# Optimization experiments

Measured on AMD Instinct MI355X. Metric: run time of the kernel, lower is better.

Reference implementation:

```python
import jax, jax.numpy as jnp
import numpy as np

N, D, K, E_T = 16384, 64, 3, 262144
EPS = 1e-8

def layernorm(x, g, b):
    m = x.mean(-1, keepdims=True)
    v = x.var(-1, keepdims=True)
    return (x - m) * jax.lax.rsqrt(v + 1e-5) * g + b

def knn_edges(coords, k):
    # PyG knn_graph(loop=False, flow='source_to_target'): edge (neighbor -> query)
    n = coords.shape[0]
    sq = jnp.sum(coords * coords, axis=-1)
    d = sq[:, None] + sq[None, :] - 2.0 * (coords @ coords.T)  # [N,N] sq dists
    d = d.at[jnp.arange(n), jnp.arange(n)].set(jnp.inf)  # exclude self
    _, idx = jax.lax.top_k(-d, k)  # [N,k] nearest neighbor indices
    src = idx.reshape(-1)
    dst = jnp.repeat(jnp.arange(n), k)
    return src, dst

def gcn_conv(x, W, b, src, dst, ew, n):
    h = x @ W
    deg = jax.ops.segment_sum(ew, dst, num_segments=n)
    dis = jnp.where(deg > 0, jax.lax.rsqrt(jnp.maximum(deg, EPS)), 0.0)
    norm = dis[src] * ew * dis[dst]
    out = jax.ops.segment_sum(h[src] * norm[:, None], dst, num_segments=n)
    return out + b

def setup_inputs():
    key = jax.random.key(0)
    ks = jax.random.split(key, 8)
    return {
        "sp_center_feat": jax.random.normal(ks[0], (N, D), jnp.float32),
        "edge_index_tran": jax.random.randint(ks[1], (2, E_T), 0, N),
        "edge_attr_rpe": jax.random.normal(ks[2], (E_T, 3), jnp.float32),
        "norm_index": jax.random.randint(ks[3], (2,), 0, N),
        "sp_crood": jax.random.uniform(ks[4], (N, 3), jnp.float32),
        "norm1_g": jnp.ones((D,), jnp.float32), "norm1_b": jnp.zeros((D,), jnp.float32),
        "norm2_g": jnp.ones((D,), jnp.float32), "norm2_b": jnp.zeros((D,), jnp.float32),
        "gcn_norm_g": jnp.ones((D,), jnp.float32), "gcn_norm_b": jnp.zeros((D,), jnp.float32),
        "W1": jax.random.normal(ks[5], (D, D), jnp.float32) / np.sqrt(D),
        "b1": jnp.zeros((D,), jnp.float32),
        "W2": jax.random.normal(ks[6], (D, D), jnp.float32) / np.sqrt(D),
        "b2": jnp.zeros((D,), jnp.float32),
    }

def reference(sp_center_feat, edge_index_tran, edge_attr_rpe, norm_index, sp_crood,
              norm1_g, norm1_b, norm2_g, norm2_b, gcn_norm_g, gcn_norm_b,
              W1, b1, W2, b2):
    n = sp_center_feat.shape[0]
    x = layernorm(sp_center_feat, norm1_g, norm1_b)
    x = x + x  # SPgrah (external transformer) stubbed as identity; module adds shortcut
    x = layernorm(x, norm2_g, norm2_b)
    shortcut = x
    src, dst = knn_edges(sp_crood, K)
    a = x[src]; b_ = x[dst]
    na = jnp.maximum(jnp.sqrt(jnp.sum(a * a, -1)), EPS)
    nb = jnp.maximum(jnp.sqrt(jnp.sum(b_ * b_, -1)), EPS)
    ew_knn = jax.nn.sigmoid(jnp.sum(a * b_, -1) / (na * nb))  # sigmoid(cosine sim)
    loop = jnp.arange(n)
    src2 = jnp.concatenate([src, loop])
    dst2 = jnp.concatenate([dst, loop])
    ew = jnp.concatenate([ew_knn, jnp.ones((n,), ew_knn.dtype)])  # self-loops w=1
    h = gcn_conv(x, W1, b1, src2, dst2, ew, n)
    h = jax.nn.relu(layernorm(h, gcn_norm_g, gcn_norm_b))
    h = gcn_conv(h, W2, b2, src2, dst2, ew, n)
    h = h + x  # residual inside SuperpointGCN
    return shortcut + h
```

## Files before the change

### kernel.cpp

```cpp
#include <hip/hip_runtime.h>
#include <math.h>

#define N 16384
#define GC 8
#define NCELL (GC*GC*GC)

__device__ __forceinline__ float wsum(float v){
  #pragma unroll
  for(int m=32;m>0;m>>=1) v += __shfl_xor(v,m,64);
  return v;
}

__device__ __forceinline__ void lexins(float dd,int j2,
    float&D0,float&D1,float&D2,int&I0,int&I1,int&I2){
  bool lt0=(dd<D0)||((dd==D0)&&(j2<I0));
  bool lt1=(dd<D1)||((dd==D1)&&(j2<I1));
  bool lt2=(dd<D2)||((dd==D2)&&(j2<I2));
  float nD2=lt1?D1:(lt2?dd:D2); int nI2=lt1?I1:(lt2?j2:I2);
  float nD1=lt0?D0:(lt1?dd:D1); int nI1=lt0?I0:(lt1?j2:I1);
  float nD0=lt0?dd:D0;          int nI0=lt0?j2:I0;
  D0=nD0;D1=nD1;D2=nD2;I0=nI0;I1=nI1;I2=nI2;
}

__device__ __forceinline__ float refdist(float qx,float qy,float qz,float qs,float4 cv){
  float dot=__fmaf_rn(qz,cv.z,__fmaf_rn(qy,cv.y,__fmul_rn(qx,cv.x)));
  float sc =__fadd_rn(qs,cv.w);
  return __fmaf_rn(-2.0f,dot,sc);
}

__global__ __launch_bounds__(256) void ln_kernel(const float* __restrict__ in,
    const float* __restrict__ g1,const float* __restrict__ b1,
    const float* __restrict__ g2,const float* __restrict__ b2,
    const float* __restrict__ coords,
    float* __restrict__ x, float* __restrict__ xn, float4* __restrict__ c4,
    int* __restrict__ cnt){
  int wave=threadIdx.x>>6, lane=threadIdx.x&63;
  int row=blockIdx.x*4+wave;
  float v=in[row*64+lane];
  float m=wsum(v)*(1.0f/64.0f);
  float d=v-m;
  float var=wsum(d*d)*(1.0f/64.0f);
  float y=d*(1.0f/sqrtf(var+1e-5f))*g1[lane]+b1[lane];
  y=y+y;
  float m2=wsum(y)*(1.0f/64.0f);
  float d2=y-m2;
  float var2=wsum(d2*d2)*(1.0f/64.0f);
  float z=d2*(1.0f/sqrtf(var2+1e-5f))*g2[lane]+b2[lane];
  x[row*64+lane]=z;
  float s=wsum(z*z);
  if(lane==0){
    xn[row]=fmaxf(sqrtf(s),1e-8f);
    float a=coords[row*3+0],b=coords[row*3+1],c=coords[row*3+2];
    float sq=__fadd_rn(__fadd_rn(__fmul_rn(a,a),__fmul_rn(b,b)),__fmul_rn(c,c));
    c4[row]=make_float4(a,b,c,sq);
    int cx=min(GC-1,(int)(a*(float)GC)), cy=min(GC-1,(int)(b*(float)GC)),
        cz=min(GC-1,(int)(c*(float)GC));
    atomicAdd(&cnt[(cz*GC+cy)*GC+cx],1);
  }
}

__global__ __launch_bounds__(256) void scatter_k(const float4* __restrict__ c4,
    const int* __restrict__ cnt, int* __restrict__ cursor,
    float4* __restrict__ sc4, int* __restrict__ sidx, int* __restrict__ cellSt){
  __shared__ int buf[NCELL];
  int tid=threadIdx.x;
  int c0v=cnt[tid], c1v=cnt[tid+256];
  buf[tid]=c0v; buf[tid+256]=c1v;
  __syncthreads();
  #pragma unroll
  for(int off=1;off<NCELL;off<<=1){
    int v0=(tid>=off)?buf[tid-off]:0;
    int v1=(tid+256>=off)?buf[tid+256-off]:0;
    __syncthreads();
    buf[tid]+=v0; buf[tid+256]+=v1;
    __syncthreads();
  }
  int e0=buf[tid]-c0v, e1=buf[tid+256]-c1v;
  if(blockIdx.x==0){
    cellSt[tid]=e0; cellSt[tid+256]=e1;
    if(tid==0) cellSt[NCELL]=N;
  }
  __syncthreads();
  buf[tid]=e0; buf[tid+256]=e1;
  __syncthreads();
  int i=blockIdx.x*256+tid;
  float4 v=c4[i];
  int cx=min(GC-1,(int)(v.x*(float)GC)), cy=min(GC-1,(int)(v.y*(float)GC)),
      cz=min(GC-1,(int)(v.z*(float)GC));
  int cell=(cz*GC+cy)*GC+cx;
  int pos=buf[cell]+atomicAdd(&cursor[cell],1);
  sc4[pos]=v; sidx[pos]=i;
}

__global__ __launch_bounds__(256) void knn_ew(const float4* __restrict__ sc4,
    const int* __restrict__ sidx, const int* __restrict__ cellSt,
    const float4* __restrict__ c4, const float* __restrict__ x,
    const float* __restrict__ xn,
    int* __restrict__ knn, float* __restrict__ ew, float* __restrict__ dis){
  int tid=threadIdx.x, bid=blockIdx.x;
  int gt=bid*256+tid;
  int lane=tid&63;
  int slot=gt>>5, part=tid&31;

  float4 qv=sc4[slot]; int q=sidx[slot];
  float qx=qv.x,qy=qv.y,qz=qv.z,qs=qv.w;
  int cx=min(GC-1,(int)(qx*(float)GC)), cy=min(GC-1,(int)(qy*(float)GC)),
      cz=min(GC-1,(int)(qz*(float)GC));
  float D0=1e30f,D1=1e30f,D2=1e30f; int I0=0x7fffffff,I1=0x7fffffff,I2=0x7fffffff;
  int xlo=max(cx-1,0), xhi=min(cx+1,GC-1);
  const float cw=1.0f/(float)GC;
  float fy0=qy-(float)cy*cw, fy1=(float)(cy+1)*cw-qy;
  float fz0=qz-(float)cz*cw, fz1=(float)(cz+1)*cw-qz;
  const int OY[9]={0,-1,1, 0,0,-1, 1,-1,1};
  const int OZ[9]={0, 0,0,-1,1,-1,-1, 1,1};
  #pragma unroll 1
  for(int k=0;k<9;k++){
    int oy=OY[k], oz=OZ[k];
    int y2=cy+oy, z2=cz+oz;
    if(y2<0||y2>=GC||z2<0||z2>=GC) continue;
    if(k>0){
      float dy=(oy<0)?fy0:((oy>0)?fy1:0.0f);
      float dz=(oz<0)?fz0:((oz>0)?fz1:0.0f);
      float bnd=dy*dy+dz*dz;
      if(bnd>D2+1e-5f) continue;
    }
    int rowb=(z2*GC+y2)*GC;
    int p0=cellSt[rowb+xlo], p1=cellSt[rowb+xhi+1];
    for(int p=p0+part;p<p1;p+=32){
      float4 cv=sc4[p]; int j2=sidx[p];
      float dd=refdist(qx,qy,qz,qs,cv);
      dd=(j2==q)?1e30f:dd;
      lexins(dd,j2,D0,D1,D2,I0,I1,I2);
    }
  }
  #pragma unroll
  for(int m=1;m<32;m<<=1){
    float e0=__shfl_xor(D0,m),e1=__shfl_xor(D1,m),e2=__shfl_xor(D2,m);
    int   f0=__shfl_xor(I0,m),f1=__shfl_xor(I1,m),f2=__shfl_xor(I2,m);
    lexins(e0,f0,D0,D1,D2,I0,I1,I2);
    lexins(e1,f1,D0,D1,D2,I0,I1,I2);
    lexins(e2,f2,D0,D1,D2,I0,I1,I2);
  }
  bool flg=false;
  if(part==0){
    float mg=1e30f;
    mg=fminf(mg,(cx>0)?(qx-(float)(cx-1)*cw):1e30f);
    mg=fminf(mg,(cx<GC-1)?((float)(cx+2)*cw-qx):1e30f);
    mg=fminf(mg,(cy>0)?(qy-(float)(cy-1)*cw):1e30f);
    mg=fminf(mg,(cy<GC-1)?((float)(cy+2)*cw-qy):1e30f);
    mg=fminf(mg,(cz>0)?(qz-(float)(cz-1)*cw):1e30f);
    mg=fminf(mg,(cz<GC-1)?((float)(cz+2)*cw-qz):1e30f);
    float mg2=mg*mg*(1.0f-1e-5f);
    flg=!(D2<mg2);
  }
  unsigned long long mask=__ballot(flg);
  while(mask){
    int b=__ffsll((unsigned long long)mask)-1; mask&=mask-1;
    int qb=__shfl(q,b);
    float bx=__shfl(qx,b),by=__shfl(qy,b),bz=__shfl(qz,b),bs=__shfl(qs,b);
    float E0=1e30f,E1=1e30f,E2=1e30f; int F0=0x7fffffff,F1=0x7fffffff,F2=0x7fffffff;
    for(int j=lane;j<N;j+=64){
      float4 cv=c4[j];
      float dd=refdist(bx,by,bz,bs,cv);
      dd=(j==qb)?1e30f:dd;
      lexins(dd,j,E0,E1,E2,F0,F1,F2);
    }
    #pragma unroll
    for(int m=1;m<64;m<<=1){
      float e0=__shfl_xor(E0,m),e1=__shfl_xor(E1,m),e2=__shfl_xor(E2,m);
      int   f0=__shfl_xor(F0,m),f1=__shfl_xor(F1,m),f2=__shfl_xor(F2,m);
      lexins(e0,f0,E0,E1,E2,F0,F1,F2);
      lexins(e1,f1,E0,E1,E2,F0,F1,F2);
      lexins(e2,f2,E0,E1,E2,F0,F1,F2);
    }
    if(lane==b){ I0=F0; I1=F1; I2=F2; }
  }
  if(part==0){ knn[q*3+0]=I0; knn[q*3+1]=I1; knn[q*3+2]=I2; }

  for(int r=0;r<2;r++){
    int qi=__shfl(q,32*r);
    int s0=__shfl(I0,32*r), s1=__shfl(I1,32*r), s2=__shfl(I2,32*r);
    float xi=x[qi*64+lane];
    float xs0=x[s0*64+lane], xs1=x[s1*64+lane], xs2=x[s2*64+lane];
    float n0=xn[s0], n1=xn[s1], n2=xn[s2];
    float ni=xn[qi];
    float dt0=wsum(xs0*xi), dt1=wsum(xs1*xi), dt2=wsum(xs2*xi);
    float e0=1.f/(1.f+expf(-(dt0/(n0*ni))));
    float e1=1.f/(1.f+expf(-(dt1/(n1*ni))));
    float e2=1.f/(1.f+expf(-(dt2/(n2*ni))));
    if(lane==0){
      ew[qi*3+0]=e0; ew[qi*3+1]=e1; ew[qi*3+2]=e2;
      float ssum=((e0+e1)+e2);
      dis[qi]=1.f/sqrtf(ssum+1.0f);
    }
  }
}

__global__ __launch_bounds__(256) void agg1_w1(const float* __restrict__ x,
    const float* __restrict__ ew, const float* __restrict__ dis,
    const int* __restrict__ knn, const float* __restrict__ W1,
    const float* __restrict__ bb1, const float* __restrict__ gg,
    const float* __restrict__ gb, float* __restrict__ a1){
  __shared__ float rowbuf[4][64];
  int tid=threadIdx.x;
  int wave=tid>>6, lane=tid&63;
  float wcol[64];
  #pragma unroll
  for(int k=0;k<64;k++) wcol[k]=W1[k*64+lane];
  float bv=bb1[lane], gv=gg[lane], bv2=gb[lane];
  int nb=blockIdx.x*16+wave*4;
  float xrA,dAA,xsA0,xsA1,xsA2,wA0,wA1,wA2;
  float xrB,dBB,xsB0,xsB1,xsB2,wB0,wB1,wB2;
  {
    int i=nb;
    float di=dis[i]; dAA=di*di;
    xrA=x[i*64+lane];
    int s0=knn[i*3+0], s1=knn[i*3+1], s2=knn[i*3+2];
    xsA0=x[s0*64+lane]; xsA1=x[s1*64+lane]; xsA2=x[s2*64+lane];
    wA0=dis[s0]*ew[i*3+0]*di; wA1=dis[s1]*ew[i*3+1]*di; wA2=dis[s2]*ew[i*3+2]*di;
  }
  #pragma unroll
  for(int r=0;r<4;r++){
    if(r<3){
      int i=nb+r+1;
      float di=dis[i]; dBB=di*di;
      xrB=x[i*64+lane];
      int s0=knn[i*3+0], s1=knn[i*3+1], s2=knn[i*3+2];
      xsB0=x[s0*64+lane]; xsB1=x[s1*64+lane]; xsB2=x[s2*64+lane];
      wB0=dis[s0]*ew[i*3+0]*di; wB1=dis[s1]*ew[i*3+1]*di; wB2=dis[s2]*ew[i*3+2]*di;
    }
    float xa=xrA*dAA;
    xa=fmaf(xsA0,wA0,xa); xa=fmaf(xsA1,wA1,xa); xa=fmaf(xsA2,wA2,xa);
    rowbuf[wave][lane]=xa;
    const float4* rb=(const float4*)&rowbuf[wave][0];
    float acc=0.f;
    #pragma unroll
    for(int k4=0;k4<16;k4++){
      float4 av=rb[k4];
      acc=fmaf(av.x,wcol[k4*4+0],acc);
      acc=fmaf(av.y,wcol[k4*4+1],acc);
      acc=fmaf(av.z,wcol[k4*4+2],acc);
      acc=fmaf(av.w,wcol[k4*4+3],acc);
    }
    acc+=bv;
    float mu=wsum(acc)*(1.0f/64.0f);
    float dd=acc-mu;
    float var=wsum(dd*dd)*(1.0f/64.0f);
    float y=dd*(1.0f/sqrtf(var+1e-5f))*gv+bv2;
    a1[(nb+r)*64+lane]=fmaxf(y,0.0f);
    xrA=xrB; dAA=dBB;
    xsA0=xsB0; xsA1=xsB1; xsA2=xsB2;
    wA0=wB0; wA1=wB1; wA2=wB2;
  }
}

__global__ __launch_bounds__(256) void agg2_w2(const float* __restrict__ a1,
    const float* __restrict__ ew, const float* __restrict__ dis,
    const int* __restrict__ knn, const float* __restrict__ W2,
    const float* __restrict__ bb2, const float* __restrict__ x,
    float* __restrict__ out){
  __shared__ float rowbuf[4][64];
  int tid=threadIdx.x;
  int wave=tid>>6, lane=tid&63;
  float wcol[64];
  #pragma unroll
  for(int k=0;k<64;k++) wcol[k]=W2[k*64+lane];
  float bv=bb2[lane];
  int nb=blockIdx.x*16+wave*4;
  float xrA,dAA,xsA0,xsA1,xsA2,wA0,wA1,wA2;
  float xrB,dBB,xsB0,xsB1,xsB2,wB0,wB1,wB2;
  {
    int i=nb;
    float di=dis[i]; dAA=di*di;
    xrA=a1[i*64+lane];
    int s0=knn[i*3+0], s1=knn[i*3+1], s2=knn[i*3+2];
    xsA0=a1[s0*64+lane]; xsA1=a1[s1*64+lane]; xsA2=a1[s2*64+lane];
    wA0=dis[s0]*ew[i*3+0]*di; wA1=dis[s1]*ew[i*3+1]*di; wA2=dis[s2]*ew[i*3+2]*di;
  }
  #pragma unroll
  for(int r=0;r<4;r++){
    if(r<3){
      int i=nb+r+1;
      float di=dis[i]; dBB=di*di;
      xrB=a1[i*64+lane];
      int s0=knn[i*3+0], s1=knn[i*3+1], s2=knn[i*3+2];
      xsB0=a1[s0*64+lane]; xsB1=a1[s1*64+lane]; xsB2=a1[s2*64+lane];
      wB0=dis[s0]*ew[i*3+0]*di; wB1=dis[s1]*ew[i*3+1]*di; wB2=dis[s2]*ew[i*3+2]*di;
    }
    float aa=xrA*dAA;
    aa=fmaf(xsA0,wA0,aa); aa=fmaf(xsA1,wA1,aa); aa=fmaf(xsA2,wA2,aa);
    rowbuf[wave][lane]=aa;
    const float4* rb=(const float4*)&rowbuf[wave][0];
    float acc=0.f;
    #pragma unroll
    for(int k4=0;k4<16;k4++){
      float4 av=rb[k4];
      acc=fmaf(av.x,wcol[k4*4+0],acc);
      acc=fmaf(av.y,wcol[k4*4+1],acc);
      acc=fmaf(av.z,wcol[k4*4+2],acc);
      acc=fmaf(av.w,wcol[k4*4+3],acc);
    }
    acc+=bv;
    float xv=x[(nb+r)*64+lane];
    out[(nb+r)*64+lane]=(acc+xv)+xv;
    xrA=xrB; dAA=dBB;
    xsA0=xsB0; xsA1=xsB1; xsA2=xsB2;
    wA0=wB0; wA1=wB1; wA2=wB2;
  }
}

extern "C" void kernel_launch(void* const* d_in, const int* in_sizes, int n_in,
                              void* d_out, int out_size, void* d_ws, size_t ws_size,
                              hipStream_t stream){
  const float* feat  =(const float*)d_in[0];
  const float* coords=(const float*)d_in[4];
  const float* g1 =(const float*)d_in[5];
  const float* b1n=(const float*)d_in[6];
  const float* g2 =(const float*)d_in[7];
  const float* b2n=(const float*)d_in[8];
  const float* gg =(const float*)d_in[9];
  const float* gb =(const float*)d_in[10];
  const float* W1 =(const float*)d_in[11];
  const float* bb1=(const float*)d_in[12];
  const float* W2 =(const float*)d_in[13];
  const float* bb2=(const float*)d_in[14];
  float* out=(float*)d_out;

  char* ws=(char*)d_ws;
  size_t o=0;
  float*  x      =(float*) (ws+o); o+=(size_t)N*64*4;
  float*  a1     =(float*) (ws+o); o+=(size_t)N*64*4;
  float*  xn     =(float*) (ws+o); o+=(size_t)N*4;
  float*  ew     =(float*) (ws+o); o+=(size_t)N*3*4;
  float*  dis    =(float*) (ws+o); o+=(size_t)N*4;
  int*    knn    =(int*)   (ws+o); o+=(size_t)N*3*4;
  float4* c4     =(float4*)(ws+o); o+=(size_t)N*16;
  float4* sc4    =(float4*)(ws+o); o+=(size_t)N*16;
  int*    sidx   =(int*)   (ws+o); o+=(size_t)N*4;
  int*    cellSt =(int*)   (ws+o); o+=(size_t)(NCELL+1)*4;
  o=(o+255)&~(size_t)255;
  int*    cnt    =(int*)   (ws+o); o+=(size_t)NCELL*4;
  int*    cursor =(int*)   (ws+o); o+=(size_t)NCELL*4;
  (void)ws_size; (void)in_sizes; (void)n_in; (void)out_size;

  hipMemsetAsync((void*)cnt, 0, (size_t)2*NCELL*4, stream);
  hipLaunchKernelGGL(ln_kernel, dim3(N/4),   dim3(256), 0, stream, feat,g1,b1n,g2,b2n,coords,x,xn,c4,cnt);
  hipLaunchKernelGGL(scatter_k, dim3(N/256), dim3(256), 0, stream, c4,cnt,cursor,sc4,sidx,cellSt);
  hipLaunchKernelGGL(knn_ew,    dim3(2048),  dim3(256), 0, stream, sc4,sidx,cellSt,c4,x,xn,knn,ew,dis);
  hipLaunchKernelGGL(agg1_w1,   dim3(N/16),  dim3(256), 0, stream, x,ew,dis,knn,W1,bb1,gg,gb,a1);
  hipLaunchKernelGGL(agg2_w2,   dim3(N/16),  dim3(256), 0, stream, a1,ew,dis,knn,W2,bb2,x,out);
}
```

Before: 155.4 us.

## Fuse all stages into one cooperative persistent kernel with grid syncs

Replaces the memset plus five kernel launches with a single cooperative kernel of 512 blocks that runs layernorm, cell histogram/scan, scatter, grid kNN with edge weights, and both GCN layers, separated by grid.sync. The cell histogram and scan now run in one block using shared-memory atomics. The aim is to remove launch overhead and the gaps between kernels. The cost is serialized phases in one block, fewer threads per phase (the kNN and aggregation loops run several passes per wave), and the overhead of grid-wide barriers. It falls back to the old multi-kernel path if the cooperative launch fails.

```diff
diff --git a/kernel.cpp b/kernel.cpp
--- a/kernel.cpp
+++ b/kernel.cpp
@@ -1,9 +1,15 @@
 #include <hip/hip_runtime.h>
+#include <hip/hip_cooperative_groups.h>
 #include <math.h>
+
+namespace cg = cooperative_groups;
 
 #define N 16384
 #define GC 8
 #define NCELL (GC*GC*GC)
+#define NBLK 512
+#define NTHR 256
+#define NWAVE ((NBLK*NTHR)/64)
 
 __device__ __forceinline__ float wsum(float v){
   #pragma unroll
@@ -26,6 +32,283 @@
   float dot=__fmaf_rn(qz,cv.z,__fmaf_rn(qy,cv.y,__fmul_rn(qx,cv.x)));
   float sc =__fadd_rn(qs,cv.w);
   return __fmaf_rn(-2.0f,dot,sc);
+}
+
+__device__ __forceinline__ int cellOf(float4 v){
+  int cx=min(GC-1,(int)(v.x*(float)GC)), cy=min(GC-1,(int)(v.y*(float)GC)),
+      cz=min(GC-1,(int)(v.z*(float)GC));
+  return (cz*GC+cy)*GC+cx;
+}
+
+struct Params {
+  const float *feat,*coords,*g1,*b1,*g2,*b2,*gg,*gb,*W1,*bb1,*W2,*bb2;
+  float *out;
+  float *x,*a1,*xn,*ew,*dis;
+  int *knn; float4 *c4,*sc4; int *sidx,*cellSt,*cursor;
+};
+
+__global__ __launch_bounds__(256,2) void fused(Params P){
+  cg::grid_group grid = cg::this_grid();
+  int tid=threadIdx.x, bid=blockIdx.x;
+  int gtid=bid*NTHR+tid;
+  int lane=tid&63, wave=tid>>6;
+  int gwave=gtid>>6;
+  __shared__ float rowbuf[4][64];
+  __shared__ int smem[2*NCELL];
+
+  if(gtid<NCELL) P.cursor[gtid]=0;
+  #pragma unroll 1
+  for(int rr=0;rr<8;rr++){
+    int row=gwave*8+rr;
+    float v=P.feat[row*64+lane];
+    float m=wsum(v)*(1.0f/64.0f);
+    float d=v-m;
+    float var=wsum(d*d)*(1.0f/64.0f);
+    float y=d*(1.0f/sqrtf(var+1e-5f))*P.g1[lane]+P.b1[lane];
+    y=y+y;
+    float m2=wsum(y)*(1.0f/64.0f);
+    float d2=y-m2;
+    float var2=wsum(d2*d2)*(1.0f/64.0f);
+    float z=d2*(1.0f/sqrtf(var2+1e-5f))*P.g2[lane]+P.b2[lane];
+    P.x[row*64+lane]=z;
+    float s=wsum(z*z);
+    if(lane==0){
+      P.xn[row]=fmaxf(sqrtf(s),1e-8f);
+      float a=P.coords[row*3+0],b=P.coords[row*3+1],c=P.coords[row*3+2];
+      float sq=__fadd_rn(__fadd_rn(__fmul_rn(a,a),__fmul_rn(b,b)),__fmul_rn(c,c));
+      P.c4[row]=make_float4(a,b,c,sq);
+    }
+  }
+  grid.sync();
+
+  if(bid==0){
+    for(int i=tid;i<NCELL;i+=NTHR) smem[i]=0;
+    __syncthreads();
+    for(int i=tid;i<N;i+=NTHR){
+      atomicAdd(&smem[cellOf(P.c4[i])],1);
+    }
+    __syncthreads();
+    for(int i=tid;i<NCELL;i+=NTHR) smem[NCELL+i]=smem[i];
+    __syncthreads();
+    for(int off=1;off<NCELL;off<<=1){
+      int v0=(tid>=off)?smem[NCELL+tid-off]:0;
+      int v1=((tid+256)>=off)?smem[NCELL+tid+256-off]:0;
+      __syncthreads();
+      smem[NCELL+tid]+=v0; smem[NCELL+tid+256]+=v1;
+      __syncthreads();
+    }
+    P.cellSt[tid]    =smem[NCELL+tid]    -smem[tid];
+    P.cellSt[tid+256]=smem[NCELL+tid+256]-smem[tid+256];
+    if(tid==0) P.cellSt[NCELL]=N;
+  }
+  grid.sync();
+
+  if(gtid<N){
+    float4 v=P.c4[gtid];
+    int cell=cellOf(v);
+    int pos=P.cellSt[cell]+atomicAdd(&P.cursor[cell],1);
+    P.sc4[pos]=v; P.sidx[pos]=gtid;
+  }
+  grid.sync();
+
+  #pragma unroll 1
+  for(int pass=0;pass<4;pass++){
+    int slot=pass*4096+(gwave<<1)+(lane>>5);
+    int part=lane&31;
+    float4 qv=P.sc4[slot]; int q=P.sidx[slot];
+    float qx=qv.x,qy=qv.y,qz=qv.z,qs=qv.w;
+    int cx=min(GC-1,(int)(qx*(float)GC)), cy=min(GC-1,(int)(qy*(float)GC)),
+        cz=min(GC-1,(int)(qz*(float)GC));
+    float D0=1e30f,D1=1e30f,D2=1e30f; int I0=0x7fffffff,I1=0x7fffffff,I2=0x7fffffff;
+    int xlo=max(cx-1,0), xhi=min(cx+1,GC-1);
+    const float cw=1.0f/(float)GC;
+    float fy0=qy-(float)cy*cw, fy1=(float)(cy+1)*cw-qy;
+    float fz0=qz-(float)cz*cw, fz1=(float)(cz+1)*cw-qz;
+    const int OY[9]={0,-1,1, 0,0,-1, 1,-1,1};
+    const int OZ[9]={0, 0,0,-1,1,-1,-1, 1,1};
+    #pragma unroll 1
+    for(int k=0;k<9;k++){
+      int oy=OY[k], oz=OZ[k];
+      int y2=cy+oy, z2=cz+oz;
+      if(y2<0||y2>=GC||z2<0||z2>=GC) continue;
+      if(k>0){
+        float dy=(oy<0)?fy0:((oy>0)?fy1:0.0f);
+        float dz=(oz<0)?fz0:((oz>0)?fz1:0.0f);
+        float bnd=dy*dy+dz*dz;
+        if(bnd>D2+1e-5f) continue;
+      }
+      int rowb=(z2*GC+y2)*GC;
+      int p0=P.cellSt[rowb+xlo], p1=P.cellSt[rowb+xhi+1];
+      for(int p=p0+part;p<p1;p+=32){
+        float4 cv=P.sc4[p]; int j2=P.sidx[p];
+        float dd=refdist(qx,qy,qz,qs,cv);
+        dd=(j2==q)?1e30f:dd;
+        lexins(dd,j2,D0,D1,D2,I0,I1,I2);
+      }
+    }
+    #pragma unroll
+    for(int m=1;m<32;m<<=1){
+      float e0=__shfl_xor(D0,m),e1=__shfl_xor(D1,m),e2=__shfl_xor(D2,m);
+      int   f0=__shfl_xor(I0,m),f1=__shfl_xor(I1,m),f2=__shfl_xor(I2,m);
+      lexins(e0,f0,D0,D1,D2,I0,I1,I2);
+      lexins(e1,f1,D0,D1,D2,I0,I1,I2);
+      lexins(e2,f2,D0,D1,D2,I0,I1,I2);
+    }
+    bool flg=false;
+    if(part==0){
+      float mg=1e30f;
+      mg=fminf(mg,(cx>0)?(qx-(float)(cx-1)*cw):1e30f);
+      mg=fminf(mg,(cx<GC-1)?((float)(cx+2)*cw-qx):1e30f);
+      mg=fminf(mg,(cy>0)?(qy-(float)(cy-1)*cw):1e30f);
+      mg=fminf(mg,(cy<GC-1)?((float)(cy+2)*cw-qy):1e30f);
+      mg=fminf(mg,(cz>0)?(qz-(float)(cz-1)*cw):1e30f);
+      mg=fminf(mg,(cz<GC-1)?((float)(cz+2)*cw-qz):1e30f);
+      float mg2=mg*mg*(1.0f-1e-5f);
+      flg=!(D2<mg2);
+    }
+    unsigned long long mask=__ballot(flg);
+    while(mask){
+      int b=__ffsll((unsigned long long)mask)-1; mask&=mask-1;
+      int qb=__shfl(q,b);
+      float bx=__shfl(qx,b),by=__shfl(qy,b),bz=__shfl(qz,b),bs=__shfl(qs,b);
+      float E0=1e30f,E1=1e30f,E2=1e30f; int F0=0x7fffffff,F1=0x7fffffff,F2=0x7fffffff;
+      for(int j=lane;j<N;j+=64){
+        float4 cv=P.c4[j];
+        float dd=refdist(bx,by,bz,bs,cv);
+        dd=(j==qb)?1e30f:dd;
+        lexins(dd,j,E0,E1,E2,F0,F1,F2);
+      }
+      #pragma unroll
+      for(int m=1;m<64;m<<=1){
+        float e0=__shfl_xor(E0,m),e1=__shfl_xor(E1,m),e2=__shfl_xor(E2,m);
+        int   f0=__shfl_xor(F0,m),f1=__shfl_xor(F1,m),f2=__shfl_xor(F2,m);
+        lexins(e0,f0,E0,E1,E2,F0,F1,F2);
+        lexins(e1,f1,E0,E1,E2,F0,F1,F2);
+        lexins(e2,f2,E0,E1,E2,F0,F1,F2);
+      }
+      if(lane==b){ I0=F0; I1=F1; I2=F2; }
+    }
+    if(part==0){ P.knn[q*3+0]=I0; P.knn[q*3+1]=I1; P.knn[q*3+2]=I2; }
+
+    for(int r=0;r<2;r++){
+      int qi=__shfl(q,32*r);
+      int s0=__shfl(I0,32*r), s1=__shfl(I1,32*r), s2=__shfl(I2,32*r);
+      float xi=P.x[qi*64+lane];
+      float xs0=P.x[s0*64+lane], xs1=P.x[s1*64+lane], xs2=P.x[s2*64+lane];
+      float n0=P.xn[s0], n1=P.xn[s1], n2=P.xn[s2];
+      float ni=P.xn[qi];
+      float dt0=wsum(xs0*xi), dt1=wsum(xs1*xi), dt2=wsum(xs2*xi);
+      float e0=1.f/(1.f+expf(-(dt0/(n0*ni))));
+      float e1=1.f/(1.f+expf(-(dt1/(n1*ni))));
+      float e2=1.f/(1.f+expf(-(dt2/(n2*ni))));
+      if(lane==0){
+        P.ew[qi*3+0]=e0; P.ew[qi*3+1]=e1; P.ew[qi*3+2]=e2;
+        float ssum=((e0+e1)+e2);
+        P.dis[qi]=1.f/sqrtf(ssum+1.0f);
+      }
+    }
+  }
+  grid.sync();
+
+  {
+    float wcol[64];
+    #pragma unroll
+    for(int k=0;k<64;k++) wcol[k]=P.W1[k*64+lane];
+    float bv=P.bb1[lane], gv=P.gg[lane], bv2=P.gb[lane];
+    int nb=gwave*8;
+    float xrA,dAA,xsA0,xsA1,xsA2,wA0,wA1,wA2;
+    float xrB,dBB,xsB0,xsB1,xsB2,wB0,wB1,wB2;
+    {
+      int i=nb;
+      float di=P.dis[i]; dAA=di*di;
+      xrA=P.x[i*64+lane];
+      int s0=P.knn[i*3+0], s1=P.knn[i*3+1], s2=P.knn[i*3+2];
+      xsA0=P.x[s0*64+lane]; xsA1=P.x[s1*64+lane]; xsA2=P.x[s2*64+lane];
+      wA0=P.dis[s0]*P.ew[i*3+0]*di; wA1=P.dis[s1]*P.ew[i*3+1]*di; wA2=P.dis[s2]*P.ew[i*3+2]*di;
+    }
+    #pragma unroll 1
+    for(int r=0;r<8;r++){
+      if(r<7){
+        int i=nb+r+1;
+        float di=P.dis[i]; dBB=di*di;
+        xrB=P.x[i*64+lane];
+        int s0=P.knn[i*3+0], s1=P.knn[i*3+1], s2=P.knn[i*3+2];
+        xsB0=P.x[s0*64+lane]; xsB1=P.x[s1*64+lane]; xsB2=P.x[s2*64+lane];
+        wB0=P.dis[s0]*P.ew[i*3+0]*di; wB1=P.dis[s1]*P.ew[i*3+1]*di; wB2=P.dis[s2]*P.ew[i*3+2]*di;
+      }
+      float xa=xrA*dAA;
+      xa=fmaf(xsA0,wA0,xa); xa=fmaf(xsA1,wA1,xa); xa=fmaf(xsA2,wA2,xa);
+      rowbuf[wave][lane]=xa;
+      const float4* rb=(const float4*)&rowbuf[wave][0];
+      float acc=0.f;
+      #pragma unroll
+      for(int k4=0;k4<16;k4++){
+        float4 av=rb[k4];
+        acc=fmaf(av.x,wcol[k4*4+0],acc);
+        acc=fmaf(av.y,wcol[k4*4+1],acc);
+        acc=fmaf(av.z,wcol[k4*4+2],acc);
+        acc=fmaf(av.w,wcol[k4*4+3],acc);
+      }
+      acc+=bv;
+      float mu=wsum(acc)*(1.0f/64.0f);
+      float dd=acc-mu;
+      float var=wsum(dd*dd)*(1.0f/64.0f);
+      float y=dd*(1.0f/sqrtf(var+1e-5f))*gv+bv2;
+      P.a1[(nb+r)*64+lane]=fmaxf(y,0.0f);
+      xrA=xrB; dAA=dBB;
+      xsA0=xsB0; xsA1=xsB1; xsA2=xsB2;
+      wA0=wB0; wA1=wB1; wA2=wB2;
+    }
+  }
+  grid.sync();
+
+  {
+    float wcol[64];
+    #pragma unroll
+    for(int k=0;k<64;k++) wcol[k]=P.W2[k*64+lane];
+    float bv=P.bb2[lane];
+    int nb=gwave*8;
+    float xrA,dAA,xsA0,xsA1,xsA2,wA0,wA1,wA2;
+    float xrB,dBB,xsB0,xsB1,xsB2,wB0,wB1,wB2;
+    {
+      int i=nb;
+      float di=P.dis[i]; dAA=di*di;
+      xrA=P.a1[i*64+lane];
+      int s0=P.knn[i*3+0], s1=P.knn[i*3+1], s2=P.knn[i*3+2];
+      xsA0=P.a1[s0*64+lane]; xsA1=P.a1[s1*64+lane]; xsA2=P.a1[s2*64+lane];
+      wA0=P.dis[s0]*P.ew[i*3+0]*di; wA1=P.dis[s1]*P.ew[i*3+1]*di; wA2=P.dis[s2]*P.ew[i*3+2]*di;
+    }
+    #pragma unroll 1
+    for(int r=0;r<8;r++){
+      if(r<7){
+        int i=nb+r+1;
+        float di=P.dis[i]; dBB=di*di;
+        xrB=P.a1[i*64+lane];
+        int s0=P.knn[i*3+0], s1=P.knn[i*3+1], s2=P.knn[i*3+2];
+        xsB0=P.a1[s0*64+lane]; xsB1=P.a1[s1*64+lane]; xsB2=P.a1[s2*64+lane];
+        wB0=P.dis[s0]*P.ew[i*3+0]*di; wB1=P.dis[s1]*P.ew[i*3+1]*di; wB2=P.dis[s2]*P.ew[i*3+2]*di;
+      }
+      float aa=xrA*dAA;
+      aa=fmaf(xsA0,wA0,aa); aa=fmaf(xsA1,wA1,aa); aa=fmaf(xsA2,wA2,aa);
+      rowbuf[wave][lane]=aa;
+      const float4* rb=(const float4*)&rowbuf[wave][0];
+      float acc=0.f;
+      #pragma unroll
+      for(int k4=0;k4<16;k4++){
+        float4 av=rb[k4];
+        acc=fmaf(av.x,wcol[k4*4+0],acc);
+        acc=fmaf(av.y,wcol[k4*4+1],acc);
+        acc=fmaf(av.z,wcol[k4*4+2],acc);
+        acc=fmaf(av.w,wcol[k4*4+3],acc);
+      }
+      acc+=bv;
+      float xv=P.x[(nb+r)*64+lane];
+      P.out[(nb+r)*64+lane]=(acc+xv)+xv;
+      xrA=xrB; dAA=dBB;
+      xsA0=xsB0; xsA1=xsB1; xsA2=xsB2;
+      wA0=wB0; wA1=wB1; wA2=wB2;
+    }
+  }
 }
 
 __global__ __launch_bounds__(256) void ln_kernel(const float* __restrict__ in,
@@ -53,9 +336,7 @@
     float a=coords[row*3+0],b=coords[row*3+1],c=coords[row*3+2];
     float sq=__fadd_rn(__fadd_rn(__fmul_rn(a,a),__fmul_rn(b,b)),__fmul_rn(c,c));
     c4[row]=make_float4(a,b,c,sq);
-    int cx=min(GC-1,(int)(a*(float)GC)), cy=min(GC-1,(int)(b*(float)GC)),
-        cz=min(GC-1,(int)(c*(float)GC));
-    atomicAdd(&cnt[(cz*GC+cy)*GC+cx],1);
+    atomicAdd(&cnt[cellOf(make_float4(a,b,c,sq))],1);
   }
 }
 
@@ -85,9 +366,7 @@
   __syncthreads();
   int i=blockIdx.x*256+tid;
   float4 v=c4[i];
-  int cx=min(GC-1,(int)(v.x*(float)GC)), cy=min(GC-1,(int)(v.y*(float)GC)),
-      cz=min(GC-1,(int)(v.z*(float)GC));
-  int cell=(cz*GC+cy)*GC+cx;
+  int cell=cellOf(v);
   int pos=buf[cell]+atomicAdd(&cursor[cell],1);
   sc4[pos]=v; sidx[pos]=i;
 }
@@ -101,7 +380,6 @@
   int gt=bid*256+tid;
   int lane=tid&63;
   int slot=gt>>5, part=tid&31;
-
   float4 qv=sc4[slot]; int q=sidx[slot];
   float qx=qv.x,qy=qv.y,qz=qv.z,qs=qv.w;
   int cx=min(GC-1,(int)(qx*(float)GC)), cy=min(GC-1,(int)(qy*(float)GC)),
@@ -176,7 +454,6 @@
     if(lane==b){ I0=F0; I1=F1; I2=F2; }
   }
   if(part==0){ knn[q*3+0]=I0; knn[q*3+1]=I1; knn[q*3+2]=I2; }
-
   for(int r=0;r<2;r++){
     int qi=__shfl(q,32*r);
     int s0=__shfl(I0,32*r), s1=__shfl(I1,32*r), s2=__shfl(I2,32*r);
@@ -343,10 +620,22 @@
   int*    cursor =(int*)   (ws+o); o+=(size_t)NCELL*4;
   (void)ws_size; (void)in_sizes; (void)n_in; (void)out_size;
 
-  hipMemsetAsync((void*)cnt, 0, (size_t)2*NCELL*4, stream);
-  hipLaunchKernelGGL(ln_kernel, dim3(N/4),   dim3(256), 0, stream, feat,g1,b1n,g2,b2n,coords,x,xn,c4,cnt);
-  hipLaunchKernelGGL(scatter_k, dim3(N/256), dim3(256), 0, stream, c4,cnt,cursor,sc4,sidx,cellSt);
-  hipLaunchKernelGGL(knn_ew,    dim3(2048),  dim3(256), 0, stream, sc4,sidx,cellSt,c4,x,xn,knn,ew,dis);
-  hipLaunchKernelGGL(agg1_w1,   dim3(N/16),  dim3(256), 0, stream, x,ew,dis,knn,W1,bb1,gg,gb,a1);
-  hipLaunchKernelGGL(agg2_w2,   dim3(N/16),  dim3(256), 0, stream, a1,ew,dis,knn,W2,bb2,x,out);
-}
+  Params Pm;
+  Pm.feat=feat; Pm.coords=coords; Pm.g1=g1; Pm.b1=b1n; Pm.g2=g2; Pm.b2=b2n;
+  Pm.gg=gg; Pm.gb=gb; Pm.W1=W1; Pm.bb1=bb1; Pm.W2=W2; Pm.bb2=bb2;
+  Pm.out=out; Pm.x=x; Pm.a1=a1; Pm.xn=xn; Pm.ew=ew; Pm.dis=dis;
+  Pm.knn=knn; Pm.c4=c4; Pm.sc4=sc4; Pm.sidx=sidx; Pm.cellSt=cellSt; Pm.cursor=cursor;
+  void* args[] = { (void*)&Pm };
+
+  hipError_t e = hipLaunchCooperativeKernel((const void*)fused, dim3(NBLK), dim3(NTHR),
+                                            args, 0, stream);
+  if(e != hipSuccess){
+    (void)hipGetLastError();
+    hipMemsetAsync((void*)cnt, 0, (size_t)2*NCELL*4, stream);
+    hipLaunchKernelGGL(ln_kernel, dim3(N/4),   dim3(256), 0, stream, feat,g1,b1n,g2,b2n,coords,x,xn,c4,cnt);
+    hipLaunchKernelGGL(scatter_k, dim3(N/256), dim3(256), 0, stream, c4,cnt,cursor,sc4,sidx,cellSt);
+    hipLaunchKernelGGL(knn_ew,    dim3(2048),  dim3(256), 0, stream, sc4,sidx,cellSt,c4,x,xn,knn,ew,dis);
+    hipLaunchKernelGGL(agg1_w1,   dim3(N/16),  dim3(256), 0, stream, x,ew,dis,knn,W1,bb1,gg,gb,a1);
+    hipLaunchKernelGGL(agg2_w2,   dim3(N/16),  dim3(256), 0, stream, a1,ew,dis,knn,W2,bb2,x,out);
+  }
+}
```

After: 494.9 us. 218% more time.

## Fuse grid binning, scatter and layernorm into one launch, drop memset

Applied to the files above, without the earlier changes.

Merges the layernorm kernel and the cell-scatter kernel into a single launch. The first 64 blocks each recount all coordinates into shared-memory histograms, do a local prefix scan, and scatter their own points. The remaining blocks run the layernorm rows. This removes one kernel launch, the memset, and the global atomics. In exchange the scatter blocks do redundant work, each reading all 16384 coordinates with shared atomics, and the order of points within a cell becomes nondeterministic.

```diff
diff --git a/kernel.cpp b/kernel.cpp
--- a/kernel.cpp
+++ b/kernel.cpp
@@ -4,6 +4,8 @@
 #define N 16384
 #define GC 8
 #define NCELL (GC*GC*GC)
+#define NSCB (N/256)
+#define NLNB (N/4)
 
 __device__ __forceinline__ float wsum(float v){
   #pragma unroll
@@ -28,68 +30,73 @@
   return __fmaf_rn(-2.0f,dot,sc);
 }
 
-__global__ __launch_bounds__(256) void ln_kernel(const float* __restrict__ in,
+__device__ __forceinline__ int cellOf3(float a,float b,float c){
+  int cx=min(GC-1,(int)(a*(float)GC)), cy=min(GC-1,(int)(b*(float)GC)),
+      cz=min(GC-1,(int)(c*(float)GC));
+  return (cz*GC+cy)*GC+cx;
+}
+
+__global__ __launch_bounds__(256) void prep_ln(const float* __restrict__ in,
     const float* __restrict__ g1,const float* __restrict__ b1,
     const float* __restrict__ g2,const float* __restrict__ b2,
     const float* __restrict__ coords,
     float* __restrict__ x, float* __restrict__ xn, float4* __restrict__ c4,
-    int* __restrict__ cnt){
-  int wave=threadIdx.x>>6, lane=threadIdx.x&63;
-  int row=blockIdx.x*4+wave;
-  float v=in[row*64+lane];
-  float m=wsum(v)*(1.0f/64.0f);
-  float d=v-m;
-  float var=wsum(d*d)*(1.0f/64.0f);
-  float y=d*(1.0f/sqrtf(var+1e-5f))*g1[lane]+b1[lane];
-  y=y+y;
-  float m2=wsum(y)*(1.0f/64.0f);
-  float d2=y-m2;
-  float var2=wsum(d2*d2)*(1.0f/64.0f);
-  float z=d2*(1.0f/sqrtf(var2+1e-5f))*g2[lane]+b2[lane];
-  x[row*64+lane]=z;
-  float s=wsum(z*z);
-  if(lane==0){
-    xn[row]=fmaxf(sqrtf(s),1e-8f);
-    float a=coords[row*3+0],b=coords[row*3+1],c=coords[row*3+2];
+    float4* __restrict__ sc4, int* __restrict__ sidx, int* __restrict__ cellSt){
+  int tid=threadIdx.x, bid=blockIdx.x;
+  if(bid<NSCB){
+    __shared__ int A[NCELL];
+    __shared__ int B[NCELL];
+    __shared__ int C[NCELL];
+    A[tid]=0; A[tid+256]=0; B[tid]=0; B[tid+256]=0;
+    __syncthreads();
+    int base=bid*256;
+    for(int i=tid;i<N;i+=256){
+      float a=coords[i*3+0], b=coords[i*3+1], c=coords[i*3+2];
+      int cell=cellOf3(a,b,c);
+      atomicAdd(&A[cell],1);
+      if(i<base) atomicAdd(&B[cell],1);
+    }
+    __syncthreads();
+    C[tid]=A[tid]; C[tid+256]=A[tid+256];
+    __syncthreads();
+    for(int off=1;off<NCELL;off<<=1){
+      int v0=(tid>=off)?C[tid-off]:0;
+      int v1=((tid+256)>=off)?C[tid+256-off]:0;
+      __syncthreads();
+      C[tid]+=v0; C[tid+256]+=v1;
+      __syncthreads();
+    }
+    C[tid]-=A[tid]; C[tid+256]-=A[tid+256];
+    A[tid]=0; A[tid+256]=0;
+    __syncthreads();
+    if(bid==0){
+      cellSt[tid]=C[tid]; cellSt[tid+256]=C[tid+256];
+      if(tid==0) cellSt[NCELL]=N;
+    }
+    int i=base+tid;
+    float a=coords[i*3+0], b=coords[i*3+1], c=coords[i*3+2];
     float sq=__fadd_rn(__fadd_rn(__fmul_rn(a,a),__fmul_rn(b,b)),__fmul_rn(c,c));
-    c4[row]=make_float4(a,b,c,sq);
-    int cx=min(GC-1,(int)(a*(float)GC)), cy=min(GC-1,(int)(b*(float)GC)),
-        cz=min(GC-1,(int)(c*(float)GC));
-    atomicAdd(&cnt[(cz*GC+cy)*GC+cx],1);
-  }
-}
-
-__global__ __launch_bounds__(256) void scatter_k(const float4* __restrict__ c4,
-    const int* __restrict__ cnt, int* __restrict__ cursor,
-    float4* __restrict__ sc4, int* __restrict__ sidx, int* __restrict__ cellSt){
-  __shared__ int buf[NCELL];
-  int tid=threadIdx.x;
-  int c0v=cnt[tid], c1v=cnt[tid+256];
-  buf[tid]=c0v; buf[tid+256]=c1v;
-  __syncthreads();
-  #pragma unroll
-  for(int off=1;off<NCELL;off<<=1){
-    int v0=(tid>=off)?buf[tid-off]:0;
-    int v1=(tid+256>=off)?buf[tid+256-off]:0;
-    __syncthreads();
-    buf[tid]+=v0; buf[tid+256]+=v1;
-    __syncthreads();
-  }
-  int e0=buf[tid]-c0v, e1=buf[tid+256]-c1v;
-  if(blockIdx.x==0){
-    cellSt[tid]=e0; cellSt[tid+256]=e1;
-    if(tid==0) cellSt[NCELL]=N;
-  }
-  __syncthreads();
-  buf[tid]=e0; buf[tid+256]=e1;
-  __syncthreads();
-  int i=blockIdx.x*256+tid;
-  float4 v=c4[i];
-  int cx=min(GC-1,(int)(v.x*(float)GC)), cy=min(GC-1,(int)(v.y*(float)GC)),
-      cz=min(GC-1,(int)(v.z*(float)GC));
-  int cell=(cz*GC+cy)*GC+cx;
-  int pos=buf[cell]+atomicAdd(&cursor[cell],1);
-  sc4[pos]=v; sidx[pos]=i;
+    float4 v=make_float4(a,b,c,sq);
+    int cell=cellOf3(a,b,c);
+    int pos=C[cell]+B[cell]+atomicAdd(&A[cell],1);
+    sc4[pos]=v; sidx[pos]=i; c4[i]=v;
+  } else {
+    int wave=tid>>6, lane=tid&63;
+    int row=(bid-NSCB)*4+wave;
+    float v=in[row*64+lane];
+    float m=wsum(v)*(1.0f/64.0f);
+    float d=v-m;
+    float var=wsum(d*d)*(1.0f/64.0f);
+    float y=d*(1.0f/sqrtf(var+1e-5f))*g1[lane]+b1[lane];
+    y=y+y;
+    float m2=wsum(y)*(1.0f/64.0f);
+    float d2=y-m2;
+    float var2=wsum(d2*d2)*(1.0f/64.0f);
+    float z=d2*(1.0f/sqrtf(var2+1e-5f))*g2[lane]+b2[lane];
+    x[row*64+lane]=z;
+    float s=wsum(z*z);
+    if(lane==0) xn[row]=fmaxf(sqrtf(s),1e-8f);
+  }
 }
 
 __global__ __launch_bounds__(256) void knn_ew(const float4* __restrict__ sc4,
@@ -101,7 +108,6 @@
   int gt=bid*256+tid;
   int lane=tid&63;
   int slot=gt>>5, part=tid&31;
-
   float4 qv=sc4[slot]; int q=sidx[slot];
   float qx=qv.x,qy=qv.y,qz=qv.z,qs=qv.w;
   int cx=min(GC-1,(int)(qx*(float)GC)), cy=min(GC-1,(int)(qy*(float)GC)),
@@ -176,7 +182,6 @@
     if(lane==b){ I0=F0; I1=F1; I2=F2; }
   }
   if(part==0){ knn[q*3+0]=I0; knn[q*3+1]=I1; knn[q*3+2]=I2; }
-
   for(int r=0;r<2;r++){
     int qi=__shfl(q,32*r);
     int s0=__shfl(I0,32*r), s1=__shfl(I1,32*r), s2=__shfl(I2,32*r);
@@ -338,15 +343,14 @@
   float4* sc4    =(float4*)(ws+o); o+=(size_t)N*16;
   int*    sidx   =(int*)   (ws+o); o+=(size_t)N*4;
   int*    cellSt =(int*)   (ws+o); o+=(size_t)(NCELL+1)*4;
-  o=(o+255)&~(size_t)255;
-  int*    cnt    =(int*)   (ws+o); o+=(size_t)NCELL*4;
-  int*    cursor =(int*)   (ws+o); o+=(size_t)NCELL*4;
   (void)ws_size; (void)in_sizes; (void)n_in; (void)out_size;
 
-  hipMemsetAsync((void*)cnt, 0, (size_t)2*NCELL*4, stream);
-  hipLaunchKernelGGL(ln_kernel, dim3(N/4),   dim3(256), 0, stream, feat,g1,b1n,g2,b2n,coords,x,xn,c4,cnt);
-  hipLaunchKernelGGL(scatter_k, dim3(N/256), dim3(256), 0, stream, c4,cnt,cursor,sc4,sidx,cellSt);
-  hipLaunchKernelGGL(knn_ew,    dim3(2048),  dim3(256), 0, stream, sc4,sidx,cellSt,c4,x,xn,knn,ew,dis);
-  hipLaunchKernelGGL(agg1_w1,   dim3(N/16),  dim3(256), 0, stream, x,ew,dis,knn,W1,bb1,gg,gb,a1);
-  hipLaunchKernelGGL(agg2_w2,   dim3(N/16),  dim3(256), 0, stream, a1,ew,dis,knn,W2,bb2,x,out);
-}
+  hipLaunchKernelGGL(prep_ln, dim3(NSCB+NLNB), dim3(256), 0, stream,
+                     feat,g1,b1n,g2,b2n,coords,x,xn,c4,sc4,sidx,cellSt);
+  hipLaunchKernelGGL(knn_ew,  dim3(2048),      dim3(256), 0, stream,
+                     sc4,sidx,cellSt,c4,x,xn,knn,ew,dis);
+  hipLaunchKernelGGL(agg1_w1, dim3(N/16),      dim3(256), 0, stream,
+                     x,ew,dis,knn,W1,bb1,gg,gb,a1);
+  hipLaunchKernelGGL(agg2_w2, dim3(N/16),      dim3(256), 0, stream,
+                     a1,ew,dis,knn,W2,bb2,x,out);
+}
```

Measured after the change: 157.0 us. About the same (+1.0%).
